# Optimization experiments

Measured on AMD Instinct MI355X. Metric: run time of the kernel, lower is better.

The kernel has to match this reference:

```python
import itertools
import jax, jax.numpy as jnp
import numpy as np


def _lin(x, w, b):
    # LogitsInference with logic_hidden_dim=[] is a single Linear (logits).
    return jnp.einsum('...i,oi->...o', x, w) + b


def _permute_cat(x, order):
    # Permutation(order): concat over all permutations of the `order` variable axes.
    if order <= 1:
        return x
    nd = x.ndim  # [B, n x order, C]
    return jnp.concatenate(
        [jnp.transpose(x, (0,) + p + (nd - 1,))
         for p in itertools.permutations(range(1, order + 1))], axis=-1)


def _expand(x, i, n):
    # Expander(i-1): insert a new object axis at position i (after existing var axes).
    x = jnp.expand_dims(x, axis=i)
    shape = list(x.shape)
    shape[i] = n
    return jnp.broadcast_to(x, tuple(shape))


def _reduce(x, order_in):
    # Reducer(order_in, exclude_self=True): mask entries with repeated indices among
    # the order_in variable axes, then take exists(max)/forall(min) over the last
    # variable axis and interleave channels -> 2*C.
    n = x.shape[1]
    if order_in >= 2:
        idx = [jnp.arange(n).reshape((1,) * k + (n,) + (1,) * (order_in - k - 1))
               for k in range(order_in)]
        mask = jnp.ones((n,) * order_in, dtype=bool)
        for a in range(order_in):
            for b in range(a + 1, order_in):
                mask = mask & (idx[a] != idx[b])
        mask = mask[None, ..., None]  # [1, n x order_in, 1]
        inp0 = jnp.where(mask, x, jnp.zeros((), x.dtype))
        inp1 = jnp.where(mask, x, jnp.ones((), x.dtype))
    else:
        inp0 = inp1 = x
    exists = jnp.max(inp0, axis=-2)
    forall = jnp.min(inp1, axis=-2)
    out = jnp.stack([exists, forall], axis=-1)  # interleave like torch stack+view
    return out.reshape(out.shape[:-2] + (out.shape[-2] * 2,))


def _bmask(act, bit, ndim):
    return act[:, bit].astype(jnp.float32).reshape((-1,) + (1,) * (ndim - 1))


def _logic_layer(x0, x1, x2, x3,
                 w_op0, b_op0, w_red0, b_red0,
                 w_exp1, b_exp1, w_op1, b_op1, w_red1, b_red1,
                 w_exp2, b_exp2, w_op2, b_op2, w_red2, b_red2,
                 w_exp3, b_exp3, w_op3, b_op3, act):
    n = x1.shape[1]
    # Per-batch-item bit masks replace index_select/index_copy_ (same math:
    # selected rows get the branch output, others contribute zero to the sum).
    # order 0: bits 0 (direct), 1 (reduce from order 1)
    s0 = (_bmask(act, 0, 2) * _lin(x0, w_op0, b_op0)
          + _bmask(act, 1, 2) * _lin(_reduce(x1, 1), w_red0, b_red0))
    o0 = jnp.where(jnp.any(act[:, 0:2] == 1), jax.nn.sigmoid(s0), jnp.zeros_like(s0))
    # order 1: bits 2 (expand from 0), 3 (direct), 4 (reduce from 2)
    s1 = (_bmask(act, 2, 3) * _lin(_expand(x0, 1, n), w_exp1, b_exp1)
          + _bmask(act, 3, 3) * _lin(x1, w_op1, b_op1)
          + _bmask(act, 4, 3) * _lin(_reduce(x2, 2), w_red1, b_red1))
    o1 = jnp.where(jnp.any(act[:, 2:5] == 1), jax.nn.sigmoid(s1), jnp.zeros_like(s1))
    # order 2: bits 5 (expand), 6 (direct), 7 (reduce)
    s2 = (_bmask(act, 5, 4) * _lin(_permute_cat(_expand(x1, 2, n), 2), w_exp2, b_exp2)
          + _bmask(act, 6, 4) * _lin(_permute_cat(x2, 2), w_op2, b_op2)
          + _bmask(act, 7, 4) * _lin(_permute_cat(_reduce(x3, 3), 2), w_red2, b_red2))
    o2 = jnp.where(jnp.any(act[:, 5:8] == 1), jax.nn.sigmoid(s2), jnp.zeros_like(s2))
    # order 3 (= max_order): bits 8 (expand), 9 (direct)
    s3 = (_bmask(act, 8, 5) * _lin(_permute_cat(_expand(x2, 3, n), 3), w_exp3, b_exp3)
          + _bmask(act, 9, 5) * _lin(_permute_cat(x3, 3), w_op3, b_op3))
    o3 = jnp.where(jnp.any(act[:, 8:10] == 1), jax.nn.sigmoid(s3), jnp.zeros_like(s3))
    return (o0, o1, o2, o3)


def setup_inputs() -> dict:
    key = jax.random.key(0)
    B, n, C, O = 8, 32, 64, 64
    ks = list(jax.random.split(key, 32))
    ki = iter(ks)
    d = {}
    d['x0'] = jax.random.normal(next(ki), (B, C), jnp.float32)
    d['x1'] = jax.random.normal(next(ki), (B, n, C), jnp.float32)
    d['x2'] = jax.random.normal(next(ki), (B, n, n, C), jnp.float32)
    d['x3'] = jax.random.normal(next(ki), (B, n, n, n, C), jnp.float32)
    in_dims = {'w_op0': C, 'w_red0': 2 * C,
               'w_exp1': C, 'w_op1': C, 'w_red1': 2 * C,
               'w_exp2': 2 * C, 'w_op2': 2 * C, 'w_red2': 4 * C,
               'w_exp3': 6 * C, 'w_op3': 6 * C}
    for name, ind in in_dims.items():
        d[name] = jax.random.normal(next(ki), (O, ind), jnp.float32) * 0.05
        d['b' + name[1:]] = jnp.zeros((O,), jnp.float32)
    d['act'] = jax.random.randint(next(ki), (B, 10), 0, 2, dtype=jnp.int32)
    return d


def reference(x0, x1, x2, x3,
              w_op0, b_op0, w_red0, b_red0,
              w_exp1, b_exp1, w_op1, b_op1, w_red1, b_red1,
              w_exp2, b_exp2, w_op2, b_op2, w_red2, b_red2,
              w_exp3, b_exp3, w_op3, b_op3, act):
    return _logic_layer(x0, x1, x2, x3,
                        w_op0, b_op0, w_red0, b_red0,
                        w_exp1, b_exp1, w_op1, b_op1, w_red1, b_red1,
                        w_exp2, b_exp2, w_op2, b_op2, w_red2, b_red2,
                        w_exp3, b_exp3, w_op3, b_op3, act)
```

## Files before the change

kernel.cpp:

```cpp
#include <hip/hip_runtime.h>
#include <hip/hip_bf16.h>
#include <math.h>

#define NB 8
#define NN 32
#define NC 64
#define NO 64

#define WS_G    0
#define WS_MF   16
#define WS_R1   128
#define WS_R2   2048
#define WS_X1B  36864
#define WS_X2B  45056
#define WS_R3B  307200
#define WS_BB   831488
#define WS_BB2  832000
#define WS_WC   832512
#define WS_WC2  1029120

typedef short bf16x8 __attribute__((ext_vector_type(8)));
typedef unsigned short u16x4 __attribute__((ext_vector_type(4)));
typedef unsigned short u16x8 __attribute__((ext_vector_type(8)));
typedef float f32x4 __attribute__((ext_vector_type(4)));

__device__ __forceinline__ float sigmoidf_(float s) {
    return 1.0f / (1.0f + expf(-s));
}

__device__ __forceinline__ unsigned short f2b(float x) {
    union { __hip_bfloat16 h; unsigned short u; } v;
    v.h = __float2bfloat16(x);
    return v.u;
}

__global__ void prep_gm(const int* __restrict__ act,
                        const float* __restrict__ be3, const float* __restrict__ bo3,
                        const float* __restrict__ be2, const float* __restrict__ bo2,
                        const float* __restrict__ br2,
                        float* __restrict__ ws) {
    int t = threadIdx.x;
    if (t < 80) ws[WS_MF + t] = (act[t] == 1) ? 1.0f : 0.0f;
    if (t < 4) {
        const int lo[4] = {0, 2, 5, 8};
        const int hi[4] = {2, 5, 8, 10};
        int any = 0;
        for (int b = 0; b < NB; ++b)
            for (int bit = lo[t]; bit < hi[t]; ++bit)
                any |= (act[b * 10 + bit] == 1);
        ws[WS_G + t] = any ? 1.0f : 0.0f;
    }
    if (t < 512) {
        int b = t >> 6, o = t & 63;
        float m8 = (act[b * 10 + 8] == 1) ? 1.0f : 0.0f;
        float m9 = (act[b * 10 + 9] == 1) ? 1.0f : 0.0f;
        ws[WS_BB + t] = m8 * be3[o] + m9 * bo3[o];
        float m5 = (act[b * 10 + 5] == 1) ? 1.0f : 0.0f;
        float m6 = (act[b * 10 + 6] == 1) ? 1.0f : 0.0f;
        float m7 = (act[b * 10 + 7] == 1) ? 1.0f : 0.0f;
        ws[WS_BB2 + t] = m5 * be2[o] + m6 * bo2[o] + m7 * br2[o];
    }
}

__global__ void prep_wc(const float* __restrict__ we3, const float* __restrict__ wo3,
                        const int* __restrict__ act, float* __restrict__ ws) {
    int tid = blockIdx.x * 256 + threadIdx.x;
    unsigned short* wc = (unsigned short*)(ws + WS_WC);
    int i8 = tid & 7;
    int lane = (tid >> 3) & 63;
    int rest = tid >> 9;
    int kk = rest % 24;
    int ntb = rest / 24;
    int nt = ntb & 3, b = ntb >> 2;
    int o = nt * 16 + (lane & 15);
    int kloc = kk * 32 + ((lane >> 4) << 3) + i8;
    bool m8 = act[b * 10 + 8] == 1;
    bool m9 = act[b * 10 + 9] == 1;
    float val;
    if (kloc < 384) val = m8 ? we3[o * 384 + kloc] : 0.0f;
    else            val = m9 ? wo3[o * 384 + kloc - 384] : 0.0f;
    wc[tid] = f2b(val);
}

__global__ void prep_wc2(const float* __restrict__ we2, const float* __restrict__ wo2,
                         const float* __restrict__ wr2, const int* __restrict__ act,
                         float* __restrict__ ws) {
    int tid = blockIdx.x * 256 + threadIdx.x;
    unsigned short* wc2 = (unsigned short*)(ws + WS_WC2);
    int i8 = tid & 7;
    int lane = (tid >> 3) & 63;
    int rest = tid >> 9;
    int kk = rest & 15;
    int ntb = rest >> 4;
    int nt = ntb & 3, b = ntb >> 2;
    int o = nt * 16 + (lane & 15);
    int kloc = kk * 32 + ((lane >> 4) << 3) + i8;
    float val;
    if (kloc < 128)      val = (act[b * 10 + 5] == 1) ? we2[o * 128 + kloc] : 0.0f;
    else if (kloc < 256) val = (act[b * 10 + 6] == 1) ? wo2[o * 128 + kloc - 128] : 0.0f;
    else                 val = (act[b * 10 + 7] == 1) ? wr2[o * 256 + kloc - 256] : 0.0f;
    wc2[tid] = f2b(val);
}

__global__ __launch_bounds__(64) void red1(const float* __restrict__ x1, float* __restrict__ ws) {
    int b = blockIdx.x, c = threadIdx.x;
    unsigned short* x1b = (unsigned short*)(ws + WS_X1B);
    float mx = -INFINITY, mn = INFINITY;
    for (int k = 0; k < NN; ++k) {
        float v = x1[(b * NN + k) * NC + c];
        x1b[(b * NN + k) * NC + c] = f2b(v);
        mx = fmaxf(mx, v); mn = fminf(mn, v);
    }
    ws[WS_R1 + b * 2 * NC + 2 * c]     = mx;
    ws[WS_R1 + b * 2 * NC + 2 * c + 1] = mn;
}

__global__ __launch_bounds__(64) void red2(const float* __restrict__ x2, float* __restrict__ ws) {
    int blk = blockIdx.x; int i = blk % NN, b = blk / NN; int c = threadIdx.x;
    unsigned short* x2b = (unsigned short*)(ws + WS_X2B);
    float mx = -INFINITY, mn = INFINITY;
    for (int jj = 0; jj < NN; ++jj) {
        float v = x2[((b * NN + i) * NN + jj) * NC + c];
        x2b[((b * NN + i) * NN + jj) * NC + c] = f2b(v);
        mx = fmaxf(mx, (jj == i) ? 0.0f : v);
        mn = fminf(mn, (jj == i) ? 1.0f : v);
    }
    ws[WS_R2 + (b * NN + i) * 2 * NC + 2 * c]     = mx;
    ws[WS_R2 + (b * NN + i) * 2 * NC + 2 * c + 1] = mn;
}

__global__ __launch_bounds__(64) void red3(const float* __restrict__ x3, float* __restrict__ ws) {
    int blk = blockIdx.x;
    int j = blk & 31, i = (blk >> 5) & 31, b = blk >> 10;
    int t = threadIdx.x;
    int kg = t >> 4, c4 = (t & 15) << 2;
    const float* base = x3 + (size_t)(((b * 32 + i) * 32 + j) * 32) * 64;
    float mx[4] = {-INFINITY, -INFINITY, -INFINITY, -INFINITY};
    float mn[4] = {INFINITY, INFINITY, INFINITY, INFINITY};
    bool alldiag = (i == j);
    #pragma unroll
    for (int it = 0; it < 8; ++it) {
        int k = it * 4 + kg;
        f32x4 v = *(const f32x4*)(base + k * 64 + c4);
        bool bad = alldiag || (k == i) || (k == j);
        #pragma unroll
        for (int q = 0; q < 4; ++q) {
            mx[q] = fmaxf(mx[q], bad ? 0.0f : v[q]);
            mn[q] = fminf(mn[q], bad ? 1.0f : v[q]);
        }
    }
    #pragma unroll
    for (int off = 16; off < 64; off <<= 1) {
        #pragma unroll
        for (int q = 0; q < 4; ++q) {
            mx[q] = fmaxf(mx[q], __shfl_xor(mx[q], off, 64));
            mn[q] = fminf(mn[q], __shfl_xor(mn[q], off, 64));
        }
    }
    if (t < 16) {
        u16x8 h;
        #pragma unroll
        for (int q = 0; q < 4; ++q) { h[2 * q] = f2b(mx[q]); h[2 * q + 1] = f2b(mn[q]); }
        unsigned short* r3b = (unsigned short*)(ws + WS_R3B);
        *(u16x8*)(r3b + (size_t)((b * 32 + i) * 32 + j) * 128 + t * 8) = h;
    }
}

__global__ __launch_bounds__(64) void out0k(
        const float* __restrict__ x0,
        const float* __restrict__ w_op0, const float* __restrict__ b_op0,
        const float* __restrict__ w_red0, const float* __restrict__ b_red0,
        const float* __restrict__ ws, float* __restrict__ out) {
    int b = blockIdx.x, o = threadIdx.x;
    float g  = ws[WS_G + 0];
    float m0 = ws[WS_MF + b * 10 + 0], m1 = ws[WS_MF + b * 10 + 1];
    float d0 = b_op0[o];
    for (int c = 0; c < NC; ++c) d0 += w_op0[o * NC + c] * x0[b * NC + c];
    float d1 = b_red0[o];
    for (int c = 0; c < 2 * NC; ++c) d1 += w_red0[o * 2 * NC + c] * ws[WS_R1 + b * 2 * NC + c];
    float s = m0 * d0 + m1 * d1;
    out[b * NO + o] = (g != 0.0f) ? sigmoidf_(s) : 0.0f;
}

__global__ __launch_bounds__(64) void out1k(
        const float* __restrict__ x0, const float* __restrict__ x1,
        const float* __restrict__ w_e1, const float* __restrict__ b_e1,
        const float* __restrict__ w_o1, const float* __restrict__ b_o1,
        const float* __restrict__ w_r1, const float* __restrict__ b_r1,
        const float* __restrict__ ws, float* __restrict__ out) {
    int blk = blockIdx.x; int i = blk % NN, b = blk / NN; int o = threadIdx.x;
    float g  = ws[WS_G + 1];
    float m2 = ws[WS_MF + b * 10 + 2];
    float m3 = ws[WS_MF + b * 10 + 3];
    float m4 = ws[WS_MF + b * 10 + 4];
    float d2 = b_e1[o];
    for (int c = 0; c < NC; ++c) d2 += w_e1[o * NC + c] * x0[b * NC + c];
    float d3 = b_o1[o];
    for (int c = 0; c < NC; ++c) d3 += w_o1[o * NC + c] * x1[(b * NN + i) * NC + c];
    float d4 = b_r1[o];
    for (int c = 0; c < 2 * NC; ++c) d4 += w_r1[o * 2 * NC + c] * ws[WS_R2 + (b * NN + i) * 2 * NC + c];
    float s = m2 * d2 + m3 * d3 + m4 * d4;
    out[(b * NN + i) * NO + o] = (g != 0.0f) ? sigmoidf_(s) : 0.0f;
}

__global__ __launch_bounds__(256) void out2k_mfma(
        const float* __restrict__ ws_f, float* __restrict__ out) {
    __shared__ unsigned short A[32 * 512];
    int blk = blockIdx.x;
    int i = blk & 31, b = blk >> 5;
    int t = threadIdx.x;
    int lane = t & 63, nt = t >> 6;
    const unsigned short* x1b = (const unsigned short*)(ws_f + WS_X1B);
    const unsigned short* x2b = (const unsigned short*)(ws_f + WS_X2B);
    const unsigned short* r3b = (const unsigned short*)(ws_f + WS_R3B);
    const unsigned short* wc2 = (const unsigned short*)(ws_f + WS_WC2);
    char* Ab = (char*)A;
    int r8 = t >> 3, c8 = (t & 7) << 3;
    {
        bf16x8 v0 = *(const bf16x8*)(x1b + (b * 32 + i) * 64 + c8);
        bf16x8 v1 = *(const bf16x8*)(x1b + b * 2048 + r8 * 64 + c8);
        bf16x8 v2 = *(const bf16x8*)(x2b + ((b * 32 + i) * 32) * 64 + r8 * 64 + c8);
        bf16x8 v3 = *(const bf16x8*)(x2b + (b * 1024 + i) * 64 + r8 * 2048 + c8);
        int sw = (r8 & 7) << 4;
        *(bf16x8*)(Ab + ((r8 * 1024 + (0 * 64 + c8) * 2) ^ sw)) = v0;
        *(bf16x8*)(Ab + ((r8 * 1024 + (1 * 64 + c8) * 2) ^ sw)) = v1;
        *(bf16x8*)(Ab + ((r8 * 1024 + (2 * 64 + c8) * 2) ^ sw)) = v2;
        *(bf16x8*)(Ab + ((r8 * 1024 + (3 * 64 + c8) * 2) ^ sw)) = v3;
    }
    int r16 = t >> 4, c16 = (t & 15) << 3;
    #pragma unroll
    for (int p = 0; p < 2; ++p) {
        int jr = p * 16 + r16;
        bf16x8 v4 = *(const bf16x8*)(r3b + ((b * 32 + i) * 32 + jr) * 128 + c16);
        bf16x8 v5 = *(const bf16x8*)(r3b + ((b * 32 + jr) * 32 + i) * 128 + c16);
        int sw = (jr & 7) << 4;
        *(bf16x8*)(Ab + ((jr * 1024 + (256 + c16) * 2) ^ sw)) = v4;
        *(bf16x8*)(Ab + ((jr * 1024 + (384 + c16) * 2) ^ sw)) = v5;
    }
    __syncthreads();
    f32x4 acc0 = {0.f, 0.f, 0.f, 0.f};
    f32x4 acc1 = {0.f, 0.f, 0.f, 0.f};
    const unsigned short* wblk = wc2 + (size_t)((b * 4 + nt) * 16) * 512 + lane * 8;
    int arow0 = lane & 15, arow1 = 16 + arow0;
    int kgrp = (lane >> 4) << 3;
    int sw0 = (arow0 & 7) << 4;
    #pragma unroll
    for (int kk = 0; kk < 16; ++kk) {
        int kloc2 = (kk * 32 + kgrp) * 2;
        bf16x8 a0 = *(const bf16x8*)(Ab + ((arow0 * 1024 + kloc2) ^ sw0));
        bf16x8 a1 = *(const bf16x8*)(Ab + ((arow1 * 1024 + kloc2) ^ sw0));
        bf16x8 bf = *(const bf16x8*)(wblk + kk * 512);
        acc0 = __builtin_amdgcn_mfma_f32_16x16x32_bf16(a0, bf, acc0, 0, 0, 0);
        acc1 = __builtin_amdgcn_mfma_f32_16x16x32_bf16(a1, bf, acc1, 0, 0, 0);
    }
    float g2 = ws_f[WS_G + 2];
    int o = nt * 16 + (lane & 15);
    float bias = ws_f[WS_BB2 + b * 64 + o];
    int rgrp = (lane >> 4) << 2;
    float* obase = out + (size_t)((b * 32 + i) * 32) * 64;
    #pragma unroll
    for (int r = 0; r < 4; ++r) {
        float s0 = acc0[r] + bias;
        float s1 = acc1[r] + bias;
        obase[(rgrp + r) * 64 + o]      = (g2 != 0.0f) ? sigmoidf_(s0) : 0.0f;
        obase[(16 + rgrp + r) * 64 + o] = (g2 != 0.0f) ? sigmoidf_(s1) : 0.0f;
    }
}

__global__ __launch_bounds__(256) void out3k_mfma(
        const float* __restrict__ x3, const float* __restrict__ ws_f,
        float* __restrict__ out) {
    __shared__ unsigned short A[32 * 768];
    int blk = blockIdx.x;
    int j = blk & 31, i = (blk >> 5) & 31, b = blk >> 10;
    int t = threadIdx.x;
    int lane = t & 63, wv = t >> 6;
    const unsigned short* x2b = (const unsigned short*)(ws_f + WS_X2B);
    const unsigned short* wc = (const unsigned short*)(ws_f + WS_WC);
    char* Ab = (char*)A;

    {
        int r8 = t >> 3, c8 = (t & 7) << 3;
        size_t cb[6]; int cs[6];
        cb[0] = ((b * 32 + i) * 32 + j) * 64; cs[0] = 0;
        cb[1] = ((b * 32 + i) * 32) * 64;     cs[1] = 64;
        cb[2] = ((b * 32 + j) * 32 + i) * 64; cs[2] = 0;
        cb[3] = (b * 1024 + i) * 64;          cs[3] = 2048;
        cb[4] = ((b * 32 + j) * 32) * 64;     cs[4] = 64;
        cb[5] = (b * 1024 + j) * 64;          cs[5] = 2048;
        int sw = (r8 & 7) << 4;
        #pragma unroll
        for (int ch = 0; ch < 6; ++ch) {
            bf16x8 v = *(const bf16x8*)(x2b + cb[ch] + (size_t)r8 * cs[ch] + c8);
            *(bf16x8*)(Ab + ((r8 * 1536 + (ch * 64 + c8) * 2) ^ sw)) = v;
        }
    }
    {
        int r16 = t >> 4, c4 = (t & 15) << 2;
        const float* xb[6]; int xs[6];
        xb[0] = x3 + (size_t)(((b * 32 + i) * 32 + j) * 32) * 64; xs[0] = 64;
        xb[1] = x3 + (size_t)(((b * 32 + i) * 32) * 32 + j) * 64; xs[1] = 2048;
        xb[2] = x3 + (size_t)(((b * 32 + j) * 32 + i) * 32) * 64; xs[2] = 64;
        xb[3] = x3 + (size_t)((b * 1024 + i) * 32 + j) * 64;      xs[3] = 65536;
        xb[4] = x3 + (size_t)(((b * 32 + j) * 32) * 32 + i) * 64; xs[4] = 2048;
        xb[5] = x3 + (size_t)(b * 32768 + j * 32 + i) * 64;       xs[5] = 65536;
        #pragma unroll
        for (int ch = 0; ch < 6; ++ch) {
            #pragma unroll
            for (int p = 0; p < 2; ++p) {
                int k = p * 16 + r16;
                f32x4 v = *(const f32x4*)(xb[ch] + (size_t)k * xs[ch] + c4);
                u16x4 h = { f2b(v[0]), f2b(v[1]), f2b(v[2]), f2b(v[3]) };
                *(u16x4*)(Ab + ((k * 1536 + ((6 + ch) * 64 + c4) * 2) ^ ((k & 7) << 4))) = h;
            }
        }
    }
    __syncthreads();

    int nt = wv;
    f32x4 acc0 = {0.f, 0.f, 0.f, 0.f};
    f32x4 acc1 = {0.f, 0.f, 0.f, 0.f};
    const unsigned short* wblk = wc + (size_t)((b * 4 + nt) * 24) * 512 + lane * 8;
    int arow0 = lane & 15;
    int arow1 = 16 + arow0;
    int kgrp = (lane >> 4) << 3;
    int sw0 = (arow0 & 7) << 4;
    #pragma unroll 4
    for (int kk = 0; kk < 24; ++kk) {
        int kloc2 = (kk * 32 + kgrp) * 2;
        bf16x8 a0 = *(const bf16x8*)(Ab + ((arow0 * 1536 + kloc2) ^ sw0));
        bf16x8 a1 = *(const bf16x8*)(Ab + ((arow1 * 1536 + kloc2) ^ sw0));
        bf16x8 bf = *(const bf16x8*)(wblk + kk * 512);
        acc0 = __builtin_amdgcn_mfma_f32_16x16x32_bf16(a0, bf, acc0, 0, 0, 0);
        acc1 = __builtin_amdgcn_mfma_f32_16x16x32_bf16(a1, bf, acc1, 0, 0, 0);
    }

    float g3 = ws_f[WS_G + 3];
    int o = nt * 16 + (lane & 15);
    float bias = ws_f[WS_BB + b * 64 + o];
    int rgrp = (lane >> 4) << 2;
    float* obase = out + (size_t)(((b * 32 + i) * 32 + j) * 32) * 64;
    #pragma unroll
    for (int r = 0; r < 4; ++r) {
        float s0 = acc0[r] + bias;
        float s1 = acc1[r] + bias;
        obase[(rgrp + r) * 64 + o]      = (g3 != 0.0f) ? sigmoidf_(s0) : 0.0f;
        obase[(16 + rgrp + r) * 64 + o] = (g3 != 0.0f) ? sigmoidf_(s1) : 0.0f;
    }
}

extern "C" void kernel_launch(void* const* d_in, const int* in_sizes, int n_in,
                              void* d_out, int out_size, void* d_ws, size_t ws_size,
                              hipStream_t stream) {
    const float* x0 = (const float*)d_in[0];
    const float* x1 = (const float*)d_in[1];
    const float* x2 = (const float*)d_in[2];
    const float* x3 = (const float*)d_in[3];
    const float* w_op0 = (const float*)d_in[4];   const float* b_op0 = (const float*)d_in[5];
    const float* w_red0 = (const float*)d_in[6];  const float* b_red0 = (const float*)d_in[7];
    const float* w_exp1 = (const float*)d_in[8];  const float* b_exp1 = (const float*)d_in[9];
    const float* w_op1 = (const float*)d_in[10];  const float* b_op1 = (const float*)d_in[11];
    const float* w_red1 = (const float*)d_in[12]; const float* b_red1 = (const float*)d_in[13];
    const float* w_exp2 = (const float*)d_in[14]; const float* b_exp2 = (const float*)d_in[15];
    const float* w_op2 = (const float*)d_in[16];  const float* b_op2 = (const float*)d_in[17];
    const float* w_red2 = (const float*)d_in[18]; const float* b_red2 = (const float*)d_in[19];
    const float* w_exp3 = (const float*)d_in[20]; const float* b_exp3 = (const float*)d_in[21];
    const float* w_op3 = (const float*)d_in[22];  const float* b_op3 = (const float*)d_in[23];
    const int* act = (const int*)d_in[24];

    float* ws = (float*)d_ws;
    float* out = (float*)d_out;
    float* out0 = out;
    float* out1 = out + 512;
    float* out2 = out + 16896;
    float* out3 = out + 541184;

    prep_gm<<<1, 512, 0, stream>>>(act, b_exp3, b_op3, b_exp2, b_op2, b_red2, ws);
    prep_wc<<<1536, 256, 0, stream>>>(w_exp3, w_op3, act, ws);
    prep_wc2<<<1024, 256, 0, stream>>>(w_exp2, w_op2, w_red2, act, ws);
    red1<<<NB, 64, 0, stream>>>(x1, ws);
    red2<<<NB * NN, 64, 0, stream>>>(x2, ws);
    red3<<<NB * NN * NN, 64, 0, stream>>>(x3, ws);
    out0k<<<NB, 64, 0, stream>>>(x0, w_op0, b_op0, w_red0, b_red0, ws, out0);
    out1k<<<NB * NN, 64, 0, stream>>>(x0, x1, w_exp1, b_exp1, w_op1, b_op1, w_red1, b_red1, ws, out1);
    out2k_mfma<<<NB * NN, 256, 0, stream>>>(ws, out2);
    out3k_mfma<<<NB * NN * NN, 256, 0, stream>>>(x3, ws, out3);
}
```

Baseline: 256.9 us.

## Merge prep kernels, move order-1 output to MFMA, halve out3 LDS footprint

Fuses the three prep kernels into one launch that also packs order-1 weights and x0 into bf16 and builds per-batch bias. Replaces the scalar out1k with an MFMA kernel that uses bf16 reduced x2 stats written by red2. Splits out3k's LDS staging into two 16-row halves, halving shared memory per block to raise occupancy, at the cost of extra barriers and serialized staging. Precision of the order-1 path drops to bf16.

```diff
diff --git a/kernel.cpp b/kernel.cpp
--- a/kernel.cpp
+++ b/kernel.cpp
@@ -18,6 +18,10 @@
 #define WS_BB2  832000
 #define WS_WC   832512
 #define WS_WC2  1029120
+#define WS_R2B  1160192
+#define WS_WC1  1176576
+#define WS_X0B  1242112
+#define WS_BB1  1242368
 
 typedef short bf16x8 __attribute__((ext_vector_type(8)));
 typedef unsigned short u16x4 __attribute__((ext_vector_type(4)));
@@ -34,72 +38,95 @@
     return v.u;
 }
 
-__global__ void prep_gm(const int* __restrict__ act,
-                        const float* __restrict__ be3, const float* __restrict__ bo3,
-                        const float* __restrict__ be2, const float* __restrict__ bo2,
-                        const float* __restrict__ br2,
-                        float* __restrict__ ws) {
-    int t = threadIdx.x;
-    if (t < 80) ws[WS_MF + t] = (act[t] == 1) ? 1.0f : 0.0f;
-    if (t < 4) {
-        const int lo[4] = {0, 2, 5, 8};
-        const int hi[4] = {2, 5, 8, 10};
-        int any = 0;
-        for (int b = 0; b < NB; ++b)
-            for (int bit = lo[t]; bit < hi[t]; ++bit)
-                any |= (act[b * 10 + bit] == 1);
-        ws[WS_G + t] = any ? 1.0f : 0.0f;
-    }
-    if (t < 512) {
-        int b = t >> 6, o = t & 63;
-        float m8 = (act[b * 10 + 8] == 1) ? 1.0f : 0.0f;
-        float m9 = (act[b * 10 + 9] == 1) ? 1.0f : 0.0f;
-        ws[WS_BB + t] = m8 * be3[o] + m9 * bo3[o];
+__global__ void prep_all(const float* __restrict__ x0,
+                         const float* __restrict__ we3, const float* __restrict__ wo3,
+                         const float* __restrict__ we2, const float* __restrict__ wo2,
+                         const float* __restrict__ wr2,
+                         const float* __restrict__ we1, const float* __restrict__ wo1,
+                         const float* __restrict__ wr1,
+                         const float* __restrict__ be1, const float* __restrict__ bo1,
+                         const float* __restrict__ br1,
+                         const float* __restrict__ be2, const float* __restrict__ bo2,
+                         const float* __restrict__ br2,
+                         const float* __restrict__ be3, const float* __restrict__ bo3,
+                         const int* __restrict__ act, float* __restrict__ ws) {
+    int bb = blockIdx.x, t = threadIdx.x;
+    if (bb < 1536) {
+        int tid = bb * 256 + t;
+        unsigned short* wc = (unsigned short*)(ws + WS_WC);
+        int i8 = tid & 7;
+        int lane = (tid >> 3) & 63;
+        int rest = tid >> 9;
+        int kk = rest % 24;
+        int ntb = rest / 24;
+        int nt = ntb & 3, b = ntb >> 2;
+        int o = nt * 16 + (lane & 15);
+        int kloc = kk * 32 + ((lane >> 4) << 3) + i8;
+        bool m8 = act[b * 10 + 8] == 1;
+        bool m9 = act[b * 10 + 9] == 1;
+        float val;
+        if (kloc < 384) val = m8 ? we3[o * 384 + kloc] : 0.0f;
+        else            val = m9 ? wo3[o * 384 + kloc - 384] : 0.0f;
+        wc[tid] = f2b(val);
+    } else if (bb < 2560) {
+        int tid = (bb - 1536) * 256 + t;
+        unsigned short* wc2 = (unsigned short*)(ws + WS_WC2);
+        int i8 = tid & 7;
+        int lane = (tid >> 3) & 63;
+        int rest = tid >> 9;
+        int kk = rest & 15;
+        int ntb = rest >> 4;
+        int nt = ntb & 3, b = ntb >> 2;
+        int o = nt * 16 + (lane & 15);
+        int kloc = kk * 32 + ((lane >> 4) << 3) + i8;
+        float val;
+        if (kloc < 128)      val = (act[b * 10 + 5] == 1) ? we2[o * 128 + kloc] : 0.0f;
+        else if (kloc < 256) val = (act[b * 10 + 6] == 1) ? wo2[o * 128 + kloc - 128] : 0.0f;
+        else                 val = (act[b * 10 + 7] == 1) ? wr2[o * 256 + kloc - 256] : 0.0f;
+        wc2[tid] = f2b(val);
+    } else if (bb < 3072) {
+        int tid = (bb - 2560) * 256 + t;
+        unsigned short* wc1 = (unsigned short*)(ws + WS_WC1);
+        int i8 = tid & 7;
+        int lane = (tid >> 3) & 63;
+        int rest = tid >> 9;
+        int kk = rest & 7;
+        int ntb = rest >> 3;
+        int nt = ntb & 3, b = ntb >> 2;
+        int o = nt * 16 + (lane & 15);
+        int kloc = kk * 32 + ((lane >> 4) << 3) + i8;
+        float val;
+        if (kloc < 64)       val = (act[b * 10 + 2] == 1) ? we1[o * 64 + kloc] : 0.0f;
+        else if (kloc < 128) val = (act[b * 10 + 3] == 1) ? wo1[o * 64 + kloc - 64] : 0.0f;
+        else                 val = (act[b * 10 + 4] == 1) ? wr1[o * 128 + kloc - 128] : 0.0f;
+        wc1[tid] = f2b(val);
+    } else {
+        int t512 = (bb - 3072) * 256 + t;
+        int b = t512 >> 6, o = t512 & 63;
+        float m2 = (act[b * 10 + 2] == 1) ? 1.0f : 0.0f;
+        float m3 = (act[b * 10 + 3] == 1) ? 1.0f : 0.0f;
+        float m4 = (act[b * 10 + 4] == 1) ? 1.0f : 0.0f;
         float m5 = (act[b * 10 + 5] == 1) ? 1.0f : 0.0f;
         float m6 = (act[b * 10 + 6] == 1) ? 1.0f : 0.0f;
         float m7 = (act[b * 10 + 7] == 1) ? 1.0f : 0.0f;
-        ws[WS_BB2 + t] = m5 * be2[o] + m6 * bo2[o] + m7 * br2[o];
-    }
-}
-
-__global__ void prep_wc(const float* __restrict__ we3, const float* __restrict__ wo3,
-                        const int* __restrict__ act, float* __restrict__ ws) {
-    int tid = blockIdx.x * 256 + threadIdx.x;
-    unsigned short* wc = (unsigned short*)(ws + WS_WC);
-    int i8 = tid & 7;
-    int lane = (tid >> 3) & 63;
-    int rest = tid >> 9;
-    int kk = rest % 24;
-    int ntb = rest / 24;
-    int nt = ntb & 3, b = ntb >> 2;
-    int o = nt * 16 + (lane & 15);
-    int kloc = kk * 32 + ((lane >> 4) << 3) + i8;
-    bool m8 = act[b * 10 + 8] == 1;
-    bool m9 = act[b * 10 + 9] == 1;
-    float val;
-    if (kloc < 384) val = m8 ? we3[o * 384 + kloc] : 0.0f;
-    else            val = m9 ? wo3[o * 384 + kloc - 384] : 0.0f;
-    wc[tid] = f2b(val);
-}
-
-__global__ void prep_wc2(const float* __restrict__ we2, const float* __restrict__ wo2,
-                         const float* __restrict__ wr2, const int* __restrict__ act,
-                         float* __restrict__ ws) {
-    int tid = blockIdx.x * 256 + threadIdx.x;
-    unsigned short* wc2 = (unsigned short*)(ws + WS_WC2);
-    int i8 = tid & 7;
-    int lane = (tid >> 3) & 63;
-    int rest = tid >> 9;
-    int kk = rest & 15;
-    int ntb = rest >> 4;
-    int nt = ntb & 3, b = ntb >> 2;
-    int o = nt * 16 + (lane & 15);
-    int kloc = kk * 32 + ((lane >> 4) << 3) + i8;
-    float val;
-    if (kloc < 128)      val = (act[b * 10 + 5] == 1) ? we2[o * 128 + kloc] : 0.0f;
-    else if (kloc < 256) val = (act[b * 10 + 6] == 1) ? wo2[o * 128 + kloc - 128] : 0.0f;
-    else                 val = (act[b * 10 + 7] == 1) ? wr2[o * 256 + kloc - 256] : 0.0f;
-    wc2[tid] = f2b(val);
+        float m8 = (act[b * 10 + 8] == 1) ? 1.0f : 0.0f;
+        float m9 = (act[b * 10 + 9] == 1) ? 1.0f : 0.0f;
+        ws[WS_BB1 + t512] = m2 * be1[o] + m3 * bo1[o] + m4 * br1[o];
+        ws[WS_BB2 + t512] = m5 * be2[o] + m6 * bo2[o] + m7 * br2[o];
+        ws[WS_BB  + t512] = m8 * be3[o] + m9 * bo3[o];
+        unsigned short* x0b = (unsigned short*)(ws + WS_X0B);
+        x0b[t512] = f2b(x0[t512]);
+        if (t512 < 80) ws[WS_MF + t512] = (act[t512] == 1) ? 1.0f : 0.0f;
+        if (t512 < 4) {
+            const int lo[4] = {0, 2, 5, 8};
+            const int hi[4] = {2, 5, 8, 10};
+            int any = 0;
+            for (int bx = 0; bx < NB; ++bx)
+                for (int bit = lo[t512]; bit < hi[t512]; ++bit)
+                    any |= (act[bx * 10 + bit] == 1);
+            ws[WS_G + t512] = any ? 1.0f : 0.0f;
+        }
+    }
 }
 
 __global__ __launch_bounds__(64) void red1(const float* __restrict__ x1, float* __restrict__ ws) {
@@ -118,6 +145,7 @@
 __global__ __launch_bounds__(64) void red2(const float* __restrict__ x2, float* __restrict__ ws) {
     int blk = blockIdx.x; int i = blk % NN, b = blk / NN; int c = threadIdx.x;
     unsigned short* x2b = (unsigned short*)(ws + WS_X2B);
+    unsigned short* r2b = (unsigned short*)(ws + WS_R2B);
     float mx = -INFINITY, mn = INFINITY;
     for (int jj = 0; jj < NN; ++jj) {
         float v = x2[((b * NN + i) * NN + jj) * NC + c];
@@ -127,6 +155,8 @@
     }
     ws[WS_R2 + (b * NN + i) * 2 * NC + 2 * c]     = mx;
     ws[WS_R2 + (b * NN + i) * 2 * NC + 2 * c + 1] = mn;
+    unsigned int packed = (unsigned int)f2b(mx) | ((unsigned int)f2b(mn) << 16);
+    *(unsigned int*)(r2b + (b * NN + i) * 128 + 2 * c) = packed;
 }
 
 __global__ __launch_bounds__(64) void red3(const float* __restrict__ x3, float* __restrict__ ws) {
@@ -182,25 +212,57 @@
     out[b * NO + o] = (g != 0.0f) ? sigmoidf_(s) : 0.0f;
 }
 
-__global__ __launch_bounds__(64) void out1k(
-        const float* __restrict__ x0, const float* __restrict__ x1,
-        const float* __restrict__ w_e1, const float* __restrict__ b_e1,
-        const float* __restrict__ w_o1, const float* __restrict__ b_o1,
-        const float* __restrict__ w_r1, const float* __restrict__ b_r1,
-        const float* __restrict__ ws, float* __restrict__ out) {
-    int blk = blockIdx.x; int i = blk % NN, b = blk / NN; int o = threadIdx.x;
-    float g  = ws[WS_G + 1];
-    float m2 = ws[WS_MF + b * 10 + 2];
-    float m3 = ws[WS_MF + b * 10 + 3];
-    float m4 = ws[WS_MF + b * 10 + 4];
-    float d2 = b_e1[o];
-    for (int c = 0; c < NC; ++c) d2 += w_e1[o * NC + c] * x0[b * NC + c];
-    float d3 = b_o1[o];
-    for (int c = 0; c < NC; ++c) d3 += w_o1[o * NC + c] * x1[(b * NN + i) * NC + c];
-    float d4 = b_r1[o];
-    for (int c = 0; c < 2 * NC; ++c) d4 += w_r1[o * 2 * NC + c] * ws[WS_R2 + (b * NN + i) * 2 * NC + c];
-    float s = m2 * d2 + m3 * d3 + m4 * d4;
-    out[(b * NN + i) * NO + o] = (g != 0.0f) ? sigmoidf_(s) : 0.0f;
+__global__ __launch_bounds__(256) void out1k_mfma(
+        const float* __restrict__ ws_f, float* __restrict__ out) {
+    __shared__ unsigned short A[32 * 256];
+    int b = blockIdx.x;
+    int t = threadIdx.x;
+    int lane = t & 63, nt = t >> 6;
+    const unsigned short* x0b = (const unsigned short*)(ws_f + WS_X0B);
+    const unsigned short* x1b = (const unsigned short*)(ws_f + WS_X1B);
+    const unsigned short* r2b = (const unsigned short*)(ws_f + WS_R2B);
+    const unsigned short* wc1 = (const unsigned short*)(ws_f + WS_WC1);
+    char* Ab = (char*)A;
+    int r = t >> 3, c8 = (t & 7) << 3;
+    int sw = (r & 7) << 4;
+    {
+        bf16x8 v0 = *(const bf16x8*)(x0b + b * 64 + c8);
+        bf16x8 v1 = *(const bf16x8*)(x1b + (b * 32 + r) * 64 + c8);
+        bf16x8 v2 = *(const bf16x8*)(r2b + (b * 32 + r) * 128 + c8);
+        bf16x8 v3 = *(const bf16x8*)(r2b + (b * 32 + r) * 128 + 64 + c8);
+        *(bf16x8*)(Ab + ((r * 512 + (0 * 64 + c8) * 2) ^ sw)) = v0;
+        *(bf16x8*)(Ab + ((r * 512 + (1 * 64 + c8) * 2) ^ sw)) = v1;
+        *(bf16x8*)(Ab + ((r * 512 + (2 * 64 + c8) * 2) ^ sw)) = v2;
+        *(bf16x8*)(Ab + ((r * 512 + (3 * 64 + c8) * 2) ^ sw)) = v3;
+    }
+    __syncthreads();
+    f32x4 acc0 = {0.f, 0.f, 0.f, 0.f};
+    f32x4 acc1 = {0.f, 0.f, 0.f, 0.f};
+    const unsigned short* wblk = wc1 + (size_t)((b * 4 + nt) * 8) * 512 + lane * 8;
+    int arow0 = lane & 15, arow1 = 16 + arow0;
+    int kgrp2 = ((lane >> 4) << 3) * 2;
+    int sw0 = (arow0 & 7) << 4;
+    #pragma unroll
+    for (int kk = 0; kk < 8; ++kk) {
+        int kloc2 = kk * 64 + kgrp2;
+        bf16x8 a0 = *(const bf16x8*)(Ab + ((arow0 * 512 + kloc2) ^ sw0));
+        bf16x8 a1 = *(const bf16x8*)(Ab + ((arow1 * 512 + kloc2) ^ sw0));
+        bf16x8 bw = *(const bf16x8*)(wblk + kk * 512);
+        acc0 = __builtin_amdgcn_mfma_f32_16x16x32_bf16(a0, bw, acc0, 0, 0, 0);
+        acc1 = __builtin_amdgcn_mfma_f32_16x16x32_bf16(a1, bw, acc1, 0, 0, 0);
+    }
+    float g1 = ws_f[WS_G + 1];
+    int o = nt * 16 + (lane & 15);
+    float bias = ws_f[WS_BB1 + b * 64 + o];
+    int rgrp = (lane >> 4) << 2;
+    float* obase = out + b * 2048;
+    #pragma unroll
+    for (int rr = 0; rr < 4; ++rr) {
+        float s0 = acc0[rr] + bias;
+        float s1 = acc1[rr] + bias;
+        obase[(rgrp + rr) * 64 + o]      = (g1 != 0.0f) ? sigmoidf_(s0) : 0.0f;
+        obase[(16 + rgrp + rr) * 64 + o] = (g1 != 0.0f) ? sigmoidf_(s1) : 0.0f;
+    }
 }
 
 __global__ __launch_bounds__(256) void out2k_mfma(
@@ -242,11 +304,11 @@
     f32x4 acc1 = {0.f, 0.f, 0.f, 0.f};
     const unsigned short* wblk = wc2 + (size_t)((b * 4 + nt) * 16) * 512 + lane * 8;
     int arow0 = lane & 15, arow1 = 16 + arow0;
-    int kgrp = (lane >> 4) << 3;
+    int kgrp2 = ((lane >> 4) << 3) * 2;
     int sw0 = (arow0 & 7) << 4;
     #pragma unroll
     for (int kk = 0; kk < 16; ++kk) {
-        int kloc2 = (kk * 32 + kgrp) * 2;
+        int kloc2 = kk * 64 + kgrp2;
         bf16x8 a0 = *(const bf16x8*)(Ab + ((arow0 * 1024 + kloc2) ^ sw0));
         bf16x8 a1 = *(const bf16x8*)(Ab + ((arow1 * 1024 + kloc2) ^ sw0));
         bf16x8 bf = *(const bf16x8*)(wblk + kk * 512);
@@ -270,7 +332,7 @@
 __global__ __launch_bounds__(256) void out3k_mfma(
         const float* __restrict__ x3, const float* __restrict__ ws_f,
         float* __restrict__ out) {
-    __shared__ unsigned short A[32 * 768];
+    __shared__ unsigned short A[16 * 768];
     int blk = blockIdx.x;
     int j = blk & 31, i = (blk >> 5) & 31, b = blk >> 10;
     int t = threadIdx.x;
@@ -279,64 +341,75 @@
     const unsigned short* wc = (const unsigned short*)(ws_f + WS_WC);
     char* Ab = (char*)A;
 
-    {
-        int r8 = t >> 3, c8 = (t & 7) << 3;
-        size_t cb[6]; int cs[6];
-        cb[0] = ((b * 32 + i) * 32 + j) * 64; cs[0] = 0;
-        cb[1] = ((b * 32 + i) * 32) * 64;     cs[1] = 64;
-        cb[2] = ((b * 32 + j) * 32 + i) * 64; cs[2] = 0;
-        cb[3] = (b * 1024 + i) * 64;          cs[3] = 2048;
-        cb[4] = ((b * 32 + j) * 32) * 64;     cs[4] = 64;
-        cb[5] = (b * 1024 + j) * 64;          cs[5] = 2048;
-        int sw = (r8 & 7) << 4;
+    size_t cb[6]; int cs[6];
+    cb[0] = ((b * 32 + i) * 32 + j) * 64; cs[0] = 0;
+    cb[1] = ((b * 32 + i) * 32) * 64;     cs[1] = 64;
+    cb[2] = ((b * 32 + j) * 32 + i) * 64; cs[2] = 0;
+    cb[3] = (b * 1024 + i) * 64;          cs[3] = 2048;
+    cb[4] = ((b * 32 + j) * 32) * 64;     cs[4] = 64;
+    cb[5] = (b * 1024 + j) * 64;          cs[5] = 2048;
+    const float* xb[6]; int xs[6];
+    xb[0] = x3 + (size_t)(((b * 32 + i) * 32 + j) * 32) * 64; xs[0] = 64;
+    xb[1] = x3 + (size_t)(((b * 32 + i) * 32) * 32 + j) * 64; xs[1] = 2048;
+    xb[2] = x3 + (size_t)(((b * 32 + j) * 32 + i) * 32) * 64; xs[2] = 64;
+    xb[3] = x3 + (size_t)((b * 1024 + i) * 32 + j) * 64;      xs[3] = 65536;
+    xb[4] = x3 + (size_t)(((b * 32 + j) * 32) * 32 + i) * 64; xs[4] = 2048;
+    xb[5] = x3 + (size_t)(b * 32768 + j * 32 + i) * 64;       xs[5] = 65536;
+
+    auto stage = [&](int h) {
+        int r = t >> 3;
+        int row = r & 15;
+        int k = h * 16 + row;
+        int cset = (r >> 4) * 3;
+        int c8 = (t & 7) << 3;
+        int sw = (row & 7) << 4;
+        #pragma unroll
+        for (int cc = 0; cc < 3; ++cc) {
+            int ch = cset + cc;
+            bf16x8 v = *(const bf16x8*)(x2b + cb[ch] + (size_t)k * cs[ch] + c8);
+            *(bf16x8*)(Ab + ((row * 1536 + (ch * 64 + c8) * 2) ^ sw)) = v;
+        }
+        int row2 = t >> 4;
+        int k2 = h * 16 + row2;
+        int c4 = (t & 15) << 2;
+        int sw2 = (row2 & 7) << 4;
         #pragma unroll
         for (int ch = 0; ch < 6; ++ch) {
-            bf16x8 v = *(const bf16x8*)(x2b + cb[ch] + (size_t)r8 * cs[ch] + c8);
-            *(bf16x8*)(Ab + ((r8 * 1536 + (ch * 64 + c8) * 2) ^ sw)) = v;
+            f32x4 v = *(const f32x4*)(xb[ch] + (size_t)k2 * xs[ch] + c4);
+            u16x4 hh = { f2b(v[0]), f2b(v[1]), f2b(v[2]), f2b(v[3]) };
+            *(u16x4*)(Ab + ((row2 * 1536 + ((6 + ch) * 64 + c4) * 2) ^ sw2)) = hh;
         }
-    }
-    {
-        int r16 = t >> 4, c4 = (t & 15) << 2;
-        const float* xb[6]; int xs[6];
-        xb[0] = x3 + (size_t)(((b * 32 + i) * 32 + j) * 32) * 64; xs[0] = 64;
-        xb[1] = x3 + (size_t)(((b * 32 + i) * 32) * 32 + j) * 64; xs[1] = 2048;
-        xb[2] = x3 + (size_t)(((b * 32 + j) * 32 + i) * 32) * 64; xs[2] = 64;
-        xb[3] = x3 + (size_t)((b * 1024 + i) * 32 + j) * 64;      xs[3] = 65536;
-        xb[4] = x3 + (size_t)(((b * 32 + j) * 32) * 32 + i) * 64; xs[4] = 2048;
-        xb[5] = x3 + (size_t)(b * 32768 + j * 32 + i) * 64;       xs[5] = 65536;
-        #pragma unroll
-        for (int ch = 0; ch < 6; ++ch) {
-            #pragma unroll
-            for (int p = 0; p < 2; ++p) {
-                int k = p * 16 + r16;
-                f32x4 v = *(const f32x4*)(xb[ch] + (size_t)k * xs[ch] + c4);
-                u16x4 h = { f2b(v[0]), f2b(v[1]), f2b(v[2]), f2b(v[3]) };
-                *(u16x4*)(Ab + ((k * 1536 + ((6 + ch) * 64 + c4) * 2) ^ ((k & 7) << 4))) = h;
-            }
-        }
-    }
-    __syncthreads();
-
-    int nt = wv;
+    };
+
+    const unsigned short* wblk = wc + (size_t)((b * 4 + wv) * 24) * 512 + lane * 8;
+    int arow = lane & 15;
+    int kgrp2 = ((lane >> 4) << 3) * 2;
+    int sw0 = (arow & 7) << 4;
     f32x4 acc0 = {0.f, 0.f, 0.f, 0.f};
     f32x4 acc1 = {0.f, 0.f, 0.f, 0.f};
-    const unsigned short* wblk = wc + (size_t)((b * 4 + nt) * 24) * 512 + lane * 8;
-    int arow0 = lane & 15;
-    int arow1 = 16 + arow0;
-    int kgrp = (lane >> 4) << 3;
-    int sw0 = (arow0 & 7) << 4;
+
+    stage(0);
+    __syncthreads();
     #pragma unroll 4
     for (int kk = 0; kk < 24; ++kk) {
-        int kloc2 = (kk * 32 + kgrp) * 2;
-        bf16x8 a0 = *(const bf16x8*)(Ab + ((arow0 * 1536 + kloc2) ^ sw0));
-        bf16x8 a1 = *(const bf16x8*)(Ab + ((arow1 * 1536 + kloc2) ^ sw0));
+        int kloc2 = kk * 64 + kgrp2;
+        bf16x8 a0 = *(const bf16x8*)(Ab + ((arow * 1536 + kloc2) ^ sw0));
         bf16x8 bf = *(const bf16x8*)(wblk + kk * 512);
         acc0 = __builtin_amdgcn_mfma_f32_16x16x32_bf16(a0, bf, acc0, 0, 0, 0);
+    }
+    __syncthreads();
+    stage(1);
+    __syncthreads();
+    #pragma unroll 4
+    for (int kk = 0; kk < 24; ++kk) {
+        int kloc2 = kk * 64 + kgrp2;
+        bf16x8 a1 = *(const bf16x8*)(Ab + ((arow * 1536 + kloc2) ^ sw0));
+        bf16x8 bf = *(const bf16x8*)(wblk + kk * 512);
         acc1 = __builtin_amdgcn_mfma_f32_16x16x32_bf16(a1, bf, acc1, 0, 0, 0);
     }
 
     float g3 = ws_f[WS_G + 3];
-    int o = nt * 16 + (lane & 15);
+    int o = wv * 16 + (lane & 15);
     float bias = ws_f[WS_BB + b * 64 + o];
     int rgrp = (lane >> 4) << 2;
     float* obase = out + (size_t)(((b * 32 + i) * 32 + j) * 32) * 64;
@@ -375,14 +448,16 @@
     float* out2 = out + 16896;
     float* out3 = out + 541184;
 
-    prep_gm<<<1, 512, 0, stream>>>(act, b_exp3, b_op3, b_exp2, b_op2, b_red2, ws);
-    prep_wc<<<1536, 256, 0, stream>>>(w_exp3, w_op3, act, ws);
-    prep_wc2<<<1024, 256, 0, stream>>>(w_exp2, w_op2, w_red2, act, ws);
+    prep_all<<<3074, 256, 0, stream>>>(x0, w_exp3, w_op3, w_exp2, w_op2, w_red2,
+                                       w_exp1, w_op1, w_red1,
+                                       b_exp1, b_op1, b_red1,
+                                       b_exp2, b_op2, b_red2,
+                                       b_exp3, b_op3, act, ws);
     red1<<<NB, 64, 0, stream>>>(x1, ws);
     red2<<<NB * NN, 64, 0, stream>>>(x2, ws);
     red3<<<NB * NN * NN, 64, 0, stream>>>(x3, ws);
     out0k<<<NB, 64, 0, stream>>>(x0, w_op0, b_op0, w_red0, b_red0, ws, out0);
-    out1k<<<NB * NN, 64, 0, stream>>>(x0, x1, w_exp1, b_exp1, w_op1, b_op1, w_red1, b_red1, ws, out1);
+    out1k_mfma<<<NB, 256, 0, stream>>>(ws, out1);
     out2k_mfma<<<NB * NN, 256, 0, stream>>>(ws, out2);
     out3k_mfma<<<NB * NN * NN, 256, 0, stream>>>(x3, ws, out3);
 }
```

Measured after the change: 258.8 us. About the same (+0.8%).
